# Performance work log

Measured on AMD Instinct MI355X. Metric: run time of the kernel, lower is better.

Reference implementation:

```python
import jax, jax.numpy as jnp
import numpy as np

N_NODES = 100000


def _gcn_conv(x, W, b, src, dst, n):
    # PyG GCNConv (default): add self-loops, norm = deg^{-1/2}[src] * deg^{-1/2}[dst]
    # degree computed on target nodes (col) with unit edge weights, then
    # out[i] = sum_{(j->i)} norm_ji * (x_j @ W) + b
    loops = jnp.arange(n, dtype=src.dtype)
    s = jnp.concatenate([src, loops])
    d = jnp.concatenate([dst, loops])
    deg = jax.ops.segment_sum(jnp.ones_like(d, dtype=x.dtype), d, num_segments=n)
    dinv = jnp.where(deg > 0, jax.lax.rsqrt(deg), 0.0)
    h = x @ W                                  # [n, out_dim]
    norm = (dinv[s] * dinv[d])[:, None]        # [E+n, 1]
    msg = h[s] * norm                          # gather + scale
    out = jax.ops.segment_sum(msg, d, num_segments=n)  # scatter-add to targets
    return out + b


def setup_inputs() -> dict:
    key = jax.random.key(0)
    ks = jax.random.split(key, 4)
    x = jax.random.normal(ks[0], (N_NODES, 128), dtype=jnp.float32)
    edge_index = jax.random.randint(ks[1], (2, 1600000), 0, N_NODES, dtype=jnp.int64)
    W1 = jax.random.normal(ks[2], (128, 16), dtype=jnp.float32) * (1.0 / np.sqrt(128))
    b1 = jnp.zeros((16,), dtype=jnp.float32)
    W2 = jax.random.normal(ks[3], (16, 3), dtype=jnp.float32) * (1.0 / np.sqrt(16))
    b2 = jnp.zeros((3,), dtype=jnp.float32)
    return {"x": x, "edge_index": edge_index, "W1": W1, "b1": b1, "W2": W2, "b2": b2}


def reference(x, edge_index, W1, b1, W2, b2):
    src, dst = edge_index[0], edge_index[1]
    n = x.shape[0]
    h = _gcn_conv(x, W1, b1, src, dst, n)
    h = jax.nn.relu(h)
    # F.dropout in eval mode == identity (deterministic baseline)
    h = _gcn_conv(h, W2, b2, src, dst, n)
    return jax.nn.log_softmax(h, axis=1)
```

## Files before the change

### kernel.cpp

```cpp
#include <hip/hip_runtime.h>
#include <hip/hip_fp16.h>
#include <math.h>


#define BSH 9
#define BNODES 512
#define P1 512
#define GROWS 64
#define K2BUF 10240
#define BCAP 12288
#define EPT 16
#define EPT2 12
#define CSTR 16

struct alignas(8) Half4 { __half x, y, z, w; };

__global__ void k1b_fat(const int* __restrict__ src, const int* __restrict__ dst,
                        int* __restrict__ cursor,
                        unsigned int* __restrict__ staging,
                        const float* __restrict__ x, const float* __restrict__ W1,
                        Half4* __restrict__ g1h, int NBK, int n, int E) {
    __shared__ int smem[7432];
    int b = blockIdx.x;
    int t = threadIdx.x;
    if (b < P1) {
        int* hist  = smem;
        int* cs    = smem + 256;
        int* rbase = smem + 512;
        int* cur   = smem + 768;
        int* buf   = smem + 1024;
        int* gaddr = smem + 4224;
        int* wsum  = smem + 7424;
        hist[t] = 0; cur[t] = 0;
        __syncthreads();
        int slice = (E + P1 - 1) / P1;
        int e0 = b * slice, e1 = min(E, e0 + slice);
        int len = e1 - e0;
        int dl[EPT], sl[EPT];
        int cnt = 0;
        for (int e = e0 + t; e < e1 && cnt < EPT; e += 256, ++cnt) {
            dl[cnt] = dst[e];
            sl[cnt] = src[e];
        }
        for (int i = 0; i < cnt; ++i)
            atomicAdd(&hist[dl[i] >> BSH], 1);
        __syncthreads();
        int h = hist[t];
        int xx = h;
        #pragma unroll
        for (int o = 1; o < 64; o <<= 1) {
            int v = __shfl_up(xx, o);
            if ((t & 63) >= o) xx += v;
        }
        if ((t & 63) == 63) wsum[t >> 6] = xx;
        __syncthreads();
        int wv = t >> 6;
        #pragma unroll
        for (int i = 0; i < 4; ++i)
            if (i < wv) xx += wsum[i];
        cs[t] = xx - h;
        rbase[t] = (h > 0 && t < NBK) ? atomicAdd(&cursor[t * CSTR], h) : 0;
        __syncthreads();
        for (int i = 0; i < cnt; ++i) {
            int d = dl[i], s = sl[i];
            int k = d >> BSH;
            int tk = atomicAdd(&cur[k], 1);
            int pos = cs[k] + tk;
            buf[pos] = (s << BSH) | (d & (BNODES - 1));
            int g = rbase[k] + tk;
            gaddr[pos] = (g < BCAP) ? (k * BCAP + g) : -1;
        }
        __syncthreads();
        for (int p = t; p < len; p += 256) {
            int a = gaddr[p];
            if (a >= 0) staging[a] = (unsigned int)buf[p];
        }
    } else {
        float4* sW4 = (float4*)smem;
        for (int i = t; i < 512; i += 256) sW4[i] = ((const float4*)W1)[i];
        __syncthreads();
        int r = t >> 2, c4 = t & 3;
        int row = (b - P1) * GROWS + r;
        if (row >= n) return;
        float acc[16];
        #pragma unroll
        for (int j = 0; j < 16; ++j) acc[j] = 0.f;
        const float4* xr = (const float4*)(x + (size_t)row * 128);
        #pragma unroll
        for (int q = 0; q < 8; ++q) {
            float4 xv = xr[q * 4 + c4];
            #pragma unroll
            for (int j = 0; j < 4; ++j) {
                int k = q * 16 + c4 * 4 + j;
                float s = (j == 0) ? xv.x : (j == 1) ? xv.y : (j == 2) ? xv.z : xv.w;
                #pragma unroll
                for (int cq = 0; cq < 4; ++cq) {
                    float4 w = sW4[k * 4 + cq];
                    acc[cq * 4 + 0] += s * w.x; acc[cq * 4 + 1] += s * w.y;
                    acc[cq * 4 + 2] += s * w.z; acc[cq * 4 + 3] += s * w.w;
                }
            }
        }
        #pragma unroll
        for (int j = 0; j < 8; ++j) {
            float send = (c4 & 1) ? acc[j] : acc[j + 8];
            float recv = __shfl_xor(send, 1);
            acc[j] = ((c4 & 1) ? acc[j + 8] : acc[j]) + recv;
        }
        #pragma unroll
        for (int j = 0; j < 4; ++j) {
            float send = (c4 & 2) ? acc[j] : acc[j + 4];
            float recv = __shfl_xor(send, 2);
            acc[j] = ((c4 & 2) ? acc[j + 4] : acc[j]) + recv;
        }
        int cidx = 2 * (c4 & 1) + ((c4 & 2) >> 1);
        Half4 hh;
        hh.x = __float2half(acc[0]); hh.y = __float2half(acc[1]);
        hh.z = __float2half(acc[2]); hh.w = __float2half(acc[3]);
        g1h[(size_t)row * 4 + cidx] = hh;
    }
}

__global__ void __launch_bounds__(1024) k2_bucket(
        const unsigned int* __restrict__ staging, const int* __restrict__ cursor,
        int* __restrict__ csr, int* __restrict__ deg, float* __restrict__ dinv,
        int* __restrict__ row_start, Half4* __restrict__ g1h, int n) {
    __shared__ int lh[BNODES], sc[BNODES], lcur[BNODES], wsum[8];
    __shared__ float ldv[BNODES];
    __shared__ int buf[K2BUF];
    int kb = blockIdx.x, t = threadIdx.x;
    int node0 = kb << BSH;
    int nloc = min(BNODES, n - node0);
    int ebase = kb * BCAP;
    int ecnt = min(cursor[kb * CSTR], BCAP);
    if (t < BNODES) { lh[t] = 0; lcur[t] = 0; }
    __syncthreads();
    int el[EPT2];
    int cnt = 0;
    for (int e = t; e < ecnt && cnt < EPT2; e += 1024, ++cnt)
        el[cnt] = (int)staging[ebase + e];
    for (int i = 0; i < cnt; ++i)
        atomicAdd(&lh[el[i] & (BNODES - 1)], 1);
    __syncthreads();
    int own = (t < BNODES) ? lh[t] : 0;
    int xx = own;
    #pragma unroll
    for (int o = 1; o < 64; o <<= 1) {
        int v = __shfl_up(xx, o);
        if ((t & 63) >= o) xx += v;
    }
    if (t < BNODES && (t & 63) == 63) wsum[t >> 6] = xx;
    __syncthreads();
    if (t < BNODES) {
        int wv = t >> 6;
        #pragma unroll
        for (int i = 0; i < 8; ++i)
            if (i < wv) xx += wsum[i];
        int excl = xx - own;
        if (t < nloc) {
            deg[node0 + t] = own;
            row_start[node0 + t] = ebase + excl;
            float dv = rsqrtf((float)(own + 1));
            dinv[node0 + t] = dv;
            ldv[t] = dv;
        }
        sc[t] = excl;
    }
    __syncthreads();
    if (ecnt <= K2BUF) {
        for (int i = 0; i < cnt; ++i) {
            int p = el[i];
            int loc = p & (BNODES - 1);
            int tk = atomicAdd(&lcur[loc], 1);
            buf[sc[loc] + tk] = p >> BSH;
        }
        __syncthreads();
        for (int p = t; p < ecnt; p += 1024)
            csr[ebase + p] = buf[p];
    } else {
        for (int i = 0; i < cnt; ++i) {
            int p = el[i];
            int loc = p & (BNODES - 1);
            int tk = atomicAdd(&lcur[loc], 1);
            csr[ebase + sc[loc] + tk] = p >> BSH;
        }
    }
    for (int j = t; j < nloc * 4; j += 1024) {
        float dv = ldv[j >> 2];
        Half4 v = g1h[(size_t)node0 * 4 + j];
        v.x = __float2half(__half2float(v.x) * dv);
        v.y = __float2half(__half2float(v.y) * dv);
        v.z = __float2half(__half2float(v.z) * dv);
        v.w = __float2half(__half2float(v.w) * dv);
        g1h[(size_t)node0 * 4 + j] = v;
    }
}

__global__ void __launch_bounds__(256, 6) k_gather1(
        const uint4* __restrict__ g1q, const int* __restrict__ csr,
        const int* __restrict__ row_start, const int* __restrict__ deg,
        const float* __restrict__ dinv, const float* __restrict__ b1,
        const float* __restrict__ W2, Half4* __restrict__ g2h, int n) {
    int idx = blockIdx.x * 256 + threadIdx.x;
    int i = idx >> 2, l = idx & 3;
    if (i >= n) return;
    int off = row_start[i], dg = deg[i];
    float acc[16];
    #pragma unroll
    for (int j = 0; j < 16; ++j) acc[j] = 0.f;
    if (l == 0) {
        uint4 p0 = g1q[2 * (size_t)i], p1 = g1q[2 * (size_t)i + 1];
        const __half2* h0 = reinterpret_cast<const __half2*>(&p0);
        const __half2* h1 = reinterpret_cast<const __half2*>(&p1);
        #pragma unroll
        for (int j = 0; j < 4; ++j) {
            float2 f0 = __half22float2(h0[j]);
            float2 f1 = __half22float2(h1[j]);
            acc[2 * j] += f0.x; acc[2 * j + 1] += f0.y;
            acc[8 + 2 * j] += f1.x; acc[9 + 2 * j] += f1.y;
        }
    }
    #pragma unroll 4
    for (int k = l; k < dg; k += 4) {
        int s = csr[off + k];
        uint4 p0 = g1q[2 * (size_t)s], p1 = g1q[2 * (size_t)s + 1];
        const __half2* h0 = reinterpret_cast<const __half2*>(&p0);
        const __half2* h1 = reinterpret_cast<const __half2*>(&p1);
        #pragma unroll
        for (int j = 0; j < 4; ++j) {
            float2 f0 = __half22float2(h0[j]);
            float2 f1 = __half22float2(h1[j]);
            acc[2 * j] += f0.x; acc[2 * j + 1] += f0.y;
            acc[8 + 2 * j] += f1.x; acc[9 + 2 * j] += f1.y;
        }
    }
    #pragma unroll
    for (int j = 0; j < 8; ++j) {
        float send = (l & 1) ? acc[j] : acc[j + 8];
        float recv = __shfl_xor(send, 1);
        acc[j] = ((l & 1) ? acc[j + 8] : acc[j]) + recv;
    }
    #pragma unroll
    for (int j = 0; j < 4; ++j) {
        float send = (l & 2) ? acc[j] : acc[j + 4];
        float recv = __shfl_xor(send, 2);
        acc[j] = ((l & 2) ? acc[j + 4] : acc[j]) + recv;
    }
    int cidx = 2 * (l & 1) + ((l & 2) >> 1);
    float di = dinv[i];
    float o0 = 0.f, o1 = 0.f, o2 = 0.f;
    #pragma unroll
    for (int j = 0; j < 4; ++j) {
        int f = cidx * 4 + j;
        float z = fmaxf(0.f, di * acc[j] + b1[f]);
        o0 += z * W2[f * 3 + 0];
        o1 += z * W2[f * 3 + 1];
        o2 += z * W2[f * 3 + 2];
    }
    o0 += __shfl_xor(o0, 1); o1 += __shfl_xor(o1, 1); o2 += __shfl_xor(o2, 1);
    o0 += __shfl_xor(o0, 2); o1 += __shfl_xor(o1, 2); o2 += __shfl_xor(o2, 2);
    if (l != 0) return;
    Half4 g;
    g.x = __float2half(di * o0); g.y = __float2half(di * o1);
    g.z = __float2half(di * o2); g.w = __float2half(0.f);
    g2h[i] = g;
}

__global__ void __launch_bounds__(256, 6) k_gather2(
        const Half4* __restrict__ g2h, const int* __restrict__ csr,
        const int* __restrict__ row_start, const int* __restrict__ deg,
        const float* __restrict__ dinv, const float* __restrict__ b2,
        float* __restrict__ out, int n) {
    int idx = blockIdx.x * 256 + threadIdx.x;
    int i = idx >> 2, l = idx & 3;
    if (i >= n) return;
    int off = row_start[i], dg = deg[i];
    float v0 = 0.f, v1 = 0.f, v2 = 0.f;
    if (l == 0) {
        Half4 s = g2h[i];
        v0 = __half2float(s.x); v1 = __half2float(s.y); v2 = __half2float(s.z);
    }
    #pragma unroll 4
    for (int e = l; e < dg; e += 4) {
        int s = csr[off + e];
        Half4 g = g2h[s];
        v0 += __half2float(g.x); v1 += __half2float(g.y); v2 += __half2float(g.z);
    }
    v0 += __shfl_xor(v0, 1); v1 += __shfl_xor(v1, 1); v2 += __shfl_xor(v2, 1);
    v0 += __shfl_xor(v0, 2); v1 += __shfl_xor(v1, 2); v2 += __shfl_xor(v2, 2);
    if (l >= 3) return;
    float di = dinv[i];
    float a0 = di * v0 + b2[0];
    float a1 = di * v1 + b2[1];
    float a2 = di * v2 + b2[2];
    float m = fmaxf(a0, fmaxf(a1, a2));
    float lse = logf(expf(a0 - m) + expf(a1 - m) + expf(a2 - m));
    float r = (l == 0) ? a0 : (l == 1) ? a1 : a2;
    out[(size_t)i * 3 + l] = r - m - lse;
}

extern "C" void kernel_launch(void* const* d_in, const int* in_sizes, int n_in,
                              void* d_out, int out_size, void* d_ws, size_t ws_size,
                              hipStream_t stream) {
    const float* x  = (const float*)d_in[0];
    const int*   ei = (const int*)d_in[1];
    const float* W1 = (const float*)d_in[2];
    const float* b1 = (const float*)d_in[3];
    const float* W2 = (const float*)d_in[4];
    const float* b2 = (const float*)d_in[5];
    float* out = (float*)d_out;

    const int n = in_sizes[0] / 128;
    const int E = in_sizes[1] / 2;
    const int* src = ei;
    const int* dst = ei + E;

    const int NBK = (n + BNODES - 1) >> BSH;

    auto align = [](size_t v) { return (v + 255) & ~(size_t)255; };
    char* ws = (char*)d_ws;
    size_t o = 0;
    int* cursor   = (int*)(ws + o); o = align(o + (size_t)NBK * CSTR * 4);
    int* deg      = (int*)(ws + o); o = align(o + (size_t)n * 4);
    float* dinv   = (float*)(ws + o); o = align(o + (size_t)n * 4);
    int* row_start= (int*)(ws + o); o = align(o + (size_t)n * 4);
    unsigned int* staging = (unsigned int*)(ws + o); o = align(o + (size_t)NBK * BCAP * 4);
    int* csr      = (int*)(ws + o); o = align(o + (size_t)NBK * BCAP * 4);
    Half4* g1h    = (Half4*)(ws + o); o = align(o + (size_t)n * 4 * 8);
    Half4* g2h    = (Half4*)(ws + o); o = align(o + (size_t)n * 8);

    const int B = 256;
    int gGemm = (n + GROWS - 1) / GROWS;
    int gn4   = (4 * n + B - 1) / B;

    hipMemsetAsync(cursor, 0, (size_t)NBK * CSTR * 4, stream);
    k1b_fat<<<P1 + gGemm, B, 0, stream>>>(src, dst, cursor, staging,
                                          x, W1, g1h, NBK, n, E);
    k2_bucket<<<NBK, 1024, 0, stream>>>(staging, cursor, csr, deg, dinv, row_start, g1h, n);
    k_gather1<<<gn4, B, 0, stream>>>((const uint4*)g1h, csr, row_start, deg, dinv, b1, W2,
                                     g2h, n);
    k_gather2<<<gn4, B, 0, stream>>>(g2h, csr, row_start, deg, dinv, b2, out, n);
}
```

Baseline: 159.5 us.

## Fuse two gather kernels with a grid-wide atomic barrier

Merges the layer-1 gather/ReLU/W2 projection kernel and the layer-2 gather/log-softmax kernel into one launch. A software grid barrier (an atomic counter zeroed by the existing memset, polled with sleep) separates the two phases, and g2h is written and read with agent-scope atomics so values are visible across blocks. This removes one kernel launch and the drain/refill gap between the two gathers. The barrier is only safe if all ~1563 blocks are co-resident, which is why launch bounds are raised to 8. Otherwise it can deadlock, and the spinning and atomic loads add their own overhead.

```diff
diff --git a/kernel.cpp b/kernel.cpp
--- a/kernel.cpp
+++ b/kernel.cpp
@@ -196,95 +196,104 @@
     }
 }
 
-__global__ void __launch_bounds__(256, 6) k_gather1(
+__global__ void __launch_bounds__(256, 8) k_gather_fused(
         const uint4* __restrict__ g1q, const int* __restrict__ csr,
         const int* __restrict__ row_start, const int* __restrict__ deg,
         const float* __restrict__ dinv, const float* __restrict__ b1,
-        const float* __restrict__ W2, Half4* __restrict__ g2h, int n) {
+        const float* __restrict__ W2, const float* __restrict__ b2,
+        Half4* __restrict__ g2h, float* __restrict__ out,
+        int* __restrict__ bar, int n) {
     int idx = blockIdx.x * 256 + threadIdx.x;
     int i = idx >> 2, l = idx & 3;
-    if (i >= n) return;
-    int off = row_start[i], dg = deg[i];
-    float acc[16];
-    #pragma unroll
-    for (int j = 0; j < 16; ++j) acc[j] = 0.f;
-    if (l == 0) {
-        uint4 p0 = g1q[2 * (size_t)i], p1 = g1q[2 * (size_t)i + 1];
-        const __half2* h0 = reinterpret_cast<const __half2*>(&p0);
-        const __half2* h1 = reinterpret_cast<const __half2*>(&p1);
+    if (i < n) {
+        int off = row_start[i], dg = deg[i];
+        float acc[16];
+        #pragma unroll
+        for (int j = 0; j < 16; ++j) acc[j] = 0.f;
+        if (l == 0) {
+            uint4 p0 = g1q[2 * (size_t)i], p1 = g1q[2 * (size_t)i + 1];
+            const __half2* h0 = reinterpret_cast<const __half2*>(&p0);
+            const __half2* h1 = reinterpret_cast<const __half2*>(&p1);
+            #pragma unroll
+            for (int j = 0; j < 4; ++j) {
+                float2 f0 = __half22float2(h0[j]);
+                float2 f1 = __half22float2(h1[j]);
+                acc[2 * j] += f0.x; acc[2 * j + 1] += f0.y;
+                acc[8 + 2 * j] += f1.x; acc[9 + 2 * j] += f1.y;
+            }
+        }
+        #pragma unroll 4
+        for (int k = l; k < dg; k += 4) {
+            int s = csr[off + k];
+            uint4 p0 = g1q[2 * (size_t)s], p1 = g1q[2 * (size_t)s + 1];
+            const __half2* h0 = reinterpret_cast<const __half2*>(&p0);
+            const __half2* h1 = reinterpret_cast<const __half2*>(&p1);
+            #pragma unroll
+            for (int j = 0; j < 4; ++j) {
+                float2 f0 = __half22float2(h0[j]);
+                float2 f1 = __half22float2(h1[j]);
+                acc[2 * j] += f0.x; acc[2 * j + 1] += f0.y;
+                acc[8 + 2 * j] += f1.x; acc[9 + 2 * j] += f1.y;
+            }
+        }
+        #pragma unroll
+        for (int j = 0; j < 8; ++j) {
+            float send = (l & 1) ? acc[j] : acc[j + 8];
+            float recv = __shfl_xor(send, 1);
+            acc[j] = ((l & 1) ? acc[j + 8] : acc[j]) + recv;
+        }
         #pragma unroll
         for (int j = 0; j < 4; ++j) {
-            float2 f0 = __half22float2(h0[j]);
-            float2 f1 = __half22float2(h1[j]);
-            acc[2 * j] += f0.x; acc[2 * j + 1] += f0.y;
-            acc[8 + 2 * j] += f1.x; acc[9 + 2 * j] += f1.y;
-        }
-    }
-    #pragma unroll 4
-    for (int k = l; k < dg; k += 4) {
-        int s = csr[off + k];
-        uint4 p0 = g1q[2 * (size_t)s], p1 = g1q[2 * (size_t)s + 1];
-        const __half2* h0 = reinterpret_cast<const __half2*>(&p0);
-        const __half2* h1 = reinterpret_cast<const __half2*>(&p1);
+            float send = (l & 2) ? acc[j] : acc[j + 4];
+            float recv = __shfl_xor(send, 2);
+            acc[j] = ((l & 2) ? acc[j + 4] : acc[j]) + recv;
+        }
+        int cidx = 2 * (l & 1) + ((l & 2) >> 1);
+        float di = dinv[i];
+        float o0 = 0.f, o1 = 0.f, o2 = 0.f;
         #pragma unroll
         for (int j = 0; j < 4; ++j) {
-            float2 f0 = __half22float2(h0[j]);
-            float2 f1 = __half22float2(h1[j]);
-            acc[2 * j] += f0.x; acc[2 * j + 1] += f0.y;
-            acc[8 + 2 * j] += f1.x; acc[9 + 2 * j] += f1.y;
-        }
-    }
-    #pragma unroll
-    for (int j = 0; j < 8; ++j) {
-        float send = (l & 1) ? acc[j] : acc[j + 8];
-        float recv = __shfl_xor(send, 1);
-        acc[j] = ((l & 1) ? acc[j + 8] : acc[j]) + recv;
-    }
-    #pragma unroll
-    for (int j = 0; j < 4; ++j) {
-        float send = (l & 2) ? acc[j] : acc[j + 4];
-        float recv = __shfl_xor(send, 2);
-        acc[j] = ((l & 2) ? acc[j + 4] : acc[j]) + recv;
-    }
-    int cidx = 2 * (l & 1) + ((l & 2) >> 1);
-    float di = dinv[i];
-    float o0 = 0.f, o1 = 0.f, o2 = 0.f;
-    #pragma unroll
-    for (int j = 0; j < 4; ++j) {
-        int f = cidx * 4 + j;
-        float z = fmaxf(0.f, di * acc[j] + b1[f]);
-        o0 += z * W2[f * 3 + 0];
-        o1 += z * W2[f * 3 + 1];
-        o2 += z * W2[f * 3 + 2];
-    }
-    o0 += __shfl_xor(o0, 1); o1 += __shfl_xor(o1, 1); o2 += __shfl_xor(o2, 1);
-    o0 += __shfl_xor(o0, 2); o1 += __shfl_xor(o1, 2); o2 += __shfl_xor(o2, 2);
-    if (l != 0) return;
-    Half4 g;
-    g.x = __float2half(di * o0); g.y = __float2half(di * o1);
-    g.z = __float2half(di * o2); g.w = __float2half(0.f);
-    g2h[i] = g;
-}
-
-__global__ void __launch_bounds__(256, 6) k_gather2(
-        const Half4* __restrict__ g2h, const int* __restrict__ csr,
-        const int* __restrict__ row_start, const int* __restrict__ deg,
-        const float* __restrict__ dinv, const float* __restrict__ b2,
-        float* __restrict__ out, int n) {
-    int idx = blockIdx.x * 256 + threadIdx.x;
-    int i = idx >> 2, l = idx & 3;
+            int f = cidx * 4 + j;
+            float z = fmaxf(0.f, di * acc[j] + b1[f]);
+            o0 += z * W2[f * 3 + 0];
+            o1 += z * W2[f * 3 + 1];
+            o2 += z * W2[f * 3 + 2];
+        }
+        o0 += __shfl_xor(o0, 1); o1 += __shfl_xor(o1, 1); o2 += __shfl_xor(o2, 1);
+        o0 += __shfl_xor(o0, 2); o1 += __shfl_xor(o1, 2); o2 += __shfl_xor(o2, 2);
+        if (l == 0) {
+            union { Half4 h; unsigned long long u; } pk;
+            pk.h.x = __float2half(di * o0); pk.h.y = __float2half(di * o1);
+            pk.h.z = __float2half(di * o2); pk.h.w = __float2half(0.f);
+            __hip_atomic_store((unsigned long long*)&g2h[i], pk.u,
+                               __ATOMIC_RELEASE, __HIP_MEMORY_SCOPE_AGENT);
+        }
+    }
+    __syncthreads();
+    if (threadIdx.x == 0) {
+        __threadfence();
+        atomicAdd(bar, 1);
+        while (__hip_atomic_load(bar, __ATOMIC_ACQUIRE,
+                                 __HIP_MEMORY_SCOPE_AGENT) < (int)gridDim.x)
+            __builtin_amdgcn_s_sleep(16);
+    }
+    __syncthreads();
+    __threadfence();
     if (i >= n) return;
     int off = row_start[i], dg = deg[i];
     float v0 = 0.f, v1 = 0.f, v2 = 0.f;
+    union { Half4 h; unsigned long long u; } pk;
     if (l == 0) {
-        Half4 s = g2h[i];
-        v0 = __half2float(s.x); v1 = __half2float(s.y); v2 = __half2float(s.z);
+        pk.u = __hip_atomic_load((const unsigned long long*)&g2h[i],
+                                 __ATOMIC_RELAXED, __HIP_MEMORY_SCOPE_AGENT);
+        v0 = __half2float(pk.h.x); v1 = __half2float(pk.h.y); v2 = __half2float(pk.h.z);
     }
     #pragma unroll 4
     for (int e = l; e < dg; e += 4) {
         int s = csr[off + e];
-        Half4 g = g2h[s];
-        v0 += __half2float(g.x); v1 += __half2float(g.y); v2 += __half2float(g.z);
+        pk.u = __hip_atomic_load((const unsigned long long*)&g2h[s],
+                                 __ATOMIC_RELAXED, __HIP_MEMORY_SCOPE_AGENT);
+        v0 += __half2float(pk.h.x); v1 += __half2float(pk.h.y); v2 += __half2float(pk.h.z);
     }
     v0 += __shfl_xor(v0, 1); v1 += __shfl_xor(v1, 1); v2 += __shfl_xor(v2, 1);
     v0 += __shfl_xor(v0, 2); v1 += __shfl_xor(v1, 2); v2 += __shfl_xor(v2, 2);
@@ -320,7 +329,7 @@
     auto align = [](size_t v) { return (v + 255) & ~(size_t)255; };
     char* ws = (char*)d_ws;
     size_t o = 0;
-    int* cursor   = (int*)(ws + o); o = align(o + (size_t)NBK * CSTR * 4);
+    int* cursor   = (int*)(ws + o); o = align(o + (size_t)NBK * CSTR * 4 + 64);
     int* deg      = (int*)(ws + o); o = align(o + (size_t)n * 4);
     float* dinv   = (float*)(ws + o); o = align(o + (size_t)n * 4);
     int* row_start= (int*)(ws + o); o = align(o + (size_t)n * 4);
@@ -329,15 +338,16 @@
     Half4* g1h    = (Half4*)(ws + o); o = align(o + (size_t)n * 4 * 8);
     Half4* g2h    = (Half4*)(ws + o); o = align(o + (size_t)n * 8);
 
+    int* bar = cursor + NBK * CSTR;
+
     const int B = 256;
     int gGemm = (n + GROWS - 1) / GROWS;
     int gn4   = (4 * n + B - 1) / B;
 
-    hipMemsetAsync(cursor, 0, (size_t)NBK * CSTR * 4, stream);
+    hipMemsetAsync(cursor, 0, (size_t)NBK * CSTR * 4 + 64, stream);
     k1b_fat<<<P1 + gGemm, B, 0, stream>>>(src, dst, cursor, staging,
                                           x, W1, g1h, NBK, n, E);
     k2_bucket<<<NBK, 1024, 0, stream>>>(staging, cursor, csr, deg, dinv, row_start, g1h, n);
-    k_gather1<<<gn4, B, 0, stream>>>((const uint4*)g1h, csr, row_start, deg, dinv, b1, W2,
-                                     g2h, n);
-    k_gather2<<<gn4, B, 0, stream>>>(g2h, csr, row_start, deg, dinv, b2, out, n);
+    k_gather_fused<<<gn4, B, 0, stream>>>((const uint4*)g1h, csr, row_start, deg,
+                                          dinv, b1, W2, b2, g2h, out, bar, n);
 }
```

Result: slower. 611.3 us (+283.2%).

## Replace CSR build and gathers with bucketed shared-memory atomic aggregation

Applied to the files above, without the earlier changes.

Removes the per-bucket CSR construction (prefix scan, local sort, csr/row_start/deg arrays). Instead, each layer's aggregation runs one block per 512-node destination bucket, reading the unsorted staging edges directly and accumulating messages into shared memory with float atomics. The degree kernel now only builds a histogram for dinv and pre-scales g1h. This avoids the CSR write and read traffic and the sorting work, but adds heavy LDS atomic contention (16 atomics per edge in layer 1), runs only about 196 blocks of 1024 threads, and makes the floating-point summation order nondeterministic.

```diff
diff --git a/kernel.cpp b/kernel.cpp
--- a/kernel.cpp
+++ b/kernel.cpp
@@ -7,10 +7,8 @@
 #define BNODES 512
 #define P1 512
 #define GROWS 64
-#define K2BUF 10240
 #define BCAP 12288
 #define EPT 16
-#define EPT2 12
 #define CSTR 16
 
 struct alignas(8) Half4 { __half x, y, z, w; };
@@ -121,71 +119,28 @@
     }
 }
 
-__global__ void __launch_bounds__(1024) k2_bucket(
+__global__ void __launch_bounds__(512) k_deg(
         const unsigned int* __restrict__ staging, const int* __restrict__ cursor,
-        int* __restrict__ csr, int* __restrict__ deg, float* __restrict__ dinv,
-        int* __restrict__ row_start, Half4* __restrict__ g1h, int n) {
-    __shared__ int lh[BNODES], sc[BNODES], lcur[BNODES], wsum[8];
+        float* __restrict__ dinv, Half4* __restrict__ g1h, int n) {
+    __shared__ int hist[BNODES];
     __shared__ float ldv[BNODES];
-    __shared__ int buf[K2BUF];
     int kb = blockIdx.x, t = threadIdx.x;
     int node0 = kb << BSH;
     int nloc = min(BNODES, n - node0);
     int ebase = kb * BCAP;
     int ecnt = min(cursor[kb * CSTR], BCAP);
-    if (t < BNODES) { lh[t] = 0; lcur[t] = 0; }
-    __syncthreads();
-    int el[EPT2];
-    int cnt = 0;
-    for (int e = t; e < ecnt && cnt < EPT2; e += 1024, ++cnt)
-        el[cnt] = (int)staging[ebase + e];
-    for (int i = 0; i < cnt; ++i)
-        atomicAdd(&lh[el[i] & (BNODES - 1)], 1);
-    __syncthreads();
-    int own = (t < BNODES) ? lh[t] : 0;
-    int xx = own;
-    #pragma unroll
-    for (int o = 1; o < 64; o <<= 1) {
-        int v = __shfl_up(xx, o);
-        if ((t & 63) >= o) xx += v;
-    }
-    if (t < BNODES && (t & 63) == 63) wsum[t >> 6] = xx;
+    if (t < BNODES) hist[t] = 0;
+    __syncthreads();
+    for (int e = t; e < ecnt; e += 512)
+        atomicAdd(&hist[staging[ebase + e] & (BNODES - 1)], 1);
     __syncthreads();
     if (t < BNODES) {
-        int wv = t >> 6;
-        #pragma unroll
-        for (int i = 0; i < 8; ++i)
-            if (i < wv) xx += wsum[i];
-        int excl = xx - own;
-        if (t < nloc) {
-            deg[node0 + t] = own;
-            row_start[node0 + t] = ebase + excl;
-            float dv = rsqrtf((float)(own + 1));
-            dinv[node0 + t] = dv;
-            ldv[t] = dv;
-        }
-        sc[t] = excl;
-    }
-    __syncthreads();
-    if (ecnt <= K2BUF) {
-        for (int i = 0; i < cnt; ++i) {
-            int p = el[i];
-            int loc = p & (BNODES - 1);
-            int tk = atomicAdd(&lcur[loc], 1);
-            buf[sc[loc] + tk] = p >> BSH;
-        }
-        __syncthreads();
-        for (int p = t; p < ecnt; p += 1024)
-            csr[ebase + p] = buf[p];
-    } else {
-        for (int i = 0; i < cnt; ++i) {
-            int p = el[i];
-            int loc = p & (BNODES - 1);
-            int tk = atomicAdd(&lcur[loc], 1);
-            csr[ebase + sc[loc] + tk] = p >> BSH;
-        }
-    }
-    for (int j = t; j < nloc * 4; j += 1024) {
+        float dv = rsqrtf((float)(hist[t] + 1));
+        ldv[t] = dv;
+        if (t < nloc) dinv[node0 + t] = dv;
+    }
+    __syncthreads();
+    for (int j = t; j < nloc * 4; j += 512) {
         float dv = ldv[j >> 2];
         Half4 v = g1h[(size_t)node0 * 4 + j];
         v.x = __float2half(__half2float(v.x) * dv);
@@ -196,107 +151,107 @@
     }
 }
 
-__global__ void __launch_bounds__(256, 6) k_gather1(
-        const uint4* __restrict__ g1q, const int* __restrict__ csr,
-        const int* __restrict__ row_start, const int* __restrict__ deg,
-        const float* __restrict__ dinv, const float* __restrict__ b1,
-        const float* __restrict__ W2, Half4* __restrict__ g2h, int n) {
-    int idx = blockIdx.x * 256 + threadIdx.x;
-    int i = idx >> 2, l = idx & 3;
-    if (i >= n) return;
-    int off = row_start[i], dg = deg[i];
-    float acc[16];
-    #pragma unroll
-    for (int j = 0; j < 16; ++j) acc[j] = 0.f;
-    if (l == 0) {
+__global__ void __launch_bounds__(1024) k_l1(
+        const unsigned int* __restrict__ staging, const int* __restrict__ cursor,
+        const uint4* __restrict__ g1q, const float* __restrict__ dinv,
+        const float* __restrict__ b1, const float* __restrict__ W2,
+        Half4* __restrict__ g2h, int n) {
+    __shared__ float acc[BNODES][17];
+    int kb = blockIdx.x, t = threadIdx.x;
+    int node0 = kb << BSH;
+    int nloc = min(BNODES, n - node0);
+    int ebase = kb * BCAP;
+    int ecnt = min(cursor[kb * CSTR], BCAP);
+    for (int j = t; j < BNODES * 17; j += 1024) ((float*)acc)[j] = 0.f;
+    __syncthreads();
+    #pragma unroll 2
+    for (int e = t; e < ecnt; e += 1024) {
+        unsigned int p = staging[ebase + e];
+        int dl = p & (BNODES - 1);
+        int s  = (int)(p >> BSH);
+        uint4 p0 = g1q[2 * (size_t)s], p1 = g1q[2 * (size_t)s + 1];
+        const __half2* h0 = reinterpret_cast<const __half2*>(&p0);
+        const __half2* h1 = reinterpret_cast<const __half2*>(&p1);
+        float* a = acc[dl];
+        #pragma unroll
+        for (int j = 0; j < 4; ++j) {
+            float2 f0 = __half22float2(h0[j]);
+            float2 f1 = __half22float2(h1[j]);
+            atomicAdd(&a[2 * j],     f0.x);
+            atomicAdd(&a[2 * j + 1], f0.y);
+            atomicAdd(&a[8 + 2 * j], f1.x);
+            atomicAdd(&a[9 + 2 * j], f1.y);
+        }
+    }
+    __syncthreads();
+    if (t < nloc) {
+        int i = node0 + t;
+        float dv = dinv[i];
         uint4 p0 = g1q[2 * (size_t)i], p1 = g1q[2 * (size_t)i + 1];
         const __half2* h0 = reinterpret_cast<const __half2*>(&p0);
         const __half2* h1 = reinterpret_cast<const __half2*>(&p1);
+        float v[16];
         #pragma unroll
         for (int j = 0; j < 4; ++j) {
             float2 f0 = __half22float2(h0[j]);
             float2 f1 = __half22float2(h1[j]);
-            acc[2 * j] += f0.x; acc[2 * j + 1] += f0.y;
-            acc[8 + 2 * j] += f1.x; acc[9 + 2 * j] += f1.y;
-        }
-    }
-    #pragma unroll 4
-    for (int k = l; k < dg; k += 4) {
-        int s = csr[off + k];
-        uint4 p0 = g1q[2 * (size_t)s], p1 = g1q[2 * (size_t)s + 1];
-        const __half2* h0 = reinterpret_cast<const __half2*>(&p0);
-        const __half2* h1 = reinterpret_cast<const __half2*>(&p1);
-        #pragma unroll
-        for (int j = 0; j < 4; ++j) {
-            float2 f0 = __half22float2(h0[j]);
-            float2 f1 = __half22float2(h1[j]);
-            acc[2 * j] += f0.x; acc[2 * j + 1] += f0.y;
-            acc[8 + 2 * j] += f1.x; acc[9 + 2 * j] += f1.y;
-        }
-    }
-    #pragma unroll
-    for (int j = 0; j < 8; ++j) {
-        float send = (l & 1) ? acc[j] : acc[j + 8];
-        float recv = __shfl_xor(send, 1);
-        acc[j] = ((l & 1) ? acc[j + 8] : acc[j]) + recv;
-    }
-    #pragma unroll
-    for (int j = 0; j < 4; ++j) {
-        float send = (l & 2) ? acc[j] : acc[j + 4];
-        float recv = __shfl_xor(send, 2);
-        acc[j] = ((l & 2) ? acc[j + 4] : acc[j]) + recv;
-    }
-    int cidx = 2 * (l & 1) + ((l & 2) >> 1);
-    float di = dinv[i];
-    float o0 = 0.f, o1 = 0.f, o2 = 0.f;
-    #pragma unroll
-    for (int j = 0; j < 4; ++j) {
-        int f = cidx * 4 + j;
-        float z = fmaxf(0.f, di * acc[j] + b1[f]);
-        o0 += z * W2[f * 3 + 0];
-        o1 += z * W2[f * 3 + 1];
-        o2 += z * W2[f * 3 + 2];
-    }
-    o0 += __shfl_xor(o0, 1); o1 += __shfl_xor(o1, 1); o2 += __shfl_xor(o2, 1);
-    o0 += __shfl_xor(o0, 2); o1 += __shfl_xor(o1, 2); o2 += __shfl_xor(o2, 2);
-    if (l != 0) return;
-    Half4 g;
-    g.x = __float2half(di * o0); g.y = __float2half(di * o1);
-    g.z = __float2half(di * o2); g.w = __float2half(0.f);
-    g2h[i] = g;
-}
-
-__global__ void __launch_bounds__(256, 6) k_gather2(
-        const Half4* __restrict__ g2h, const int* __restrict__ csr,
-        const int* __restrict__ row_start, const int* __restrict__ deg,
-        const float* __restrict__ dinv, const float* __restrict__ b2,
-        float* __restrict__ out, int n) {
-    int idx = blockIdx.x * 256 + threadIdx.x;
-    int i = idx >> 2, l = idx & 3;
-    if (i >= n) return;
-    int off = row_start[i], dg = deg[i];
-    float v0 = 0.f, v1 = 0.f, v2 = 0.f;
-    if (l == 0) {
-        Half4 s = g2h[i];
-        v0 = __half2float(s.x); v1 = __half2float(s.y); v2 = __half2float(s.z);
-    }
-    #pragma unroll 4
-    for (int e = l; e < dg; e += 4) {
-        int s = csr[off + e];
+            v[2 * j]     = acc[t][2 * j]     + f0.x;
+            v[2 * j + 1] = acc[t][2 * j + 1] + f0.y;
+            v[8 + 2 * j] = acc[t][8 + 2 * j] + f1.x;
+            v[9 + 2 * j] = acc[t][9 + 2 * j] + f1.y;
+        }
+        float o0 = 0.f, o1 = 0.f, o2 = 0.f;
+        #pragma unroll
+        for (int f = 0; f < 16; ++f) {
+            float z = fmaxf(0.f, dv * v[f] + b1[f]);
+            o0 += z * W2[f * 3 + 0];
+            o1 += z * W2[f * 3 + 1];
+            o2 += z * W2[f * 3 + 2];
+        }
+        Half4 g;
+        g.x = __float2half(dv * o0); g.y = __float2half(dv * o1);
+        g.z = __float2half(dv * o2); g.w = __float2half(0.f);
+        g2h[i] = g;
+    }
+}
+
+__global__ void __launch_bounds__(1024) k_l2(
+        const unsigned int* __restrict__ staging, const int* __restrict__ cursor,
+        const Half4* __restrict__ g2h, const float* __restrict__ dinv,
+        const float* __restrict__ b2, float* __restrict__ out, int n) {
+    __shared__ float acc[BNODES][5];
+    int kb = blockIdx.x, t = threadIdx.x;
+    int node0 = kb << BSH;
+    int nloc = min(BNODES, n - node0);
+    int ebase = kb * BCAP;
+    int ecnt = min(cursor[kb * CSTR], BCAP);
+    for (int j = t; j < BNODES * 5; j += 1024) ((float*)acc)[j] = 0.f;
+    __syncthreads();
+    #pragma unroll 2
+    for (int e = t; e < ecnt; e += 1024) {
+        unsigned int p = staging[ebase + e];
+        int dl = p & (BNODES - 1);
+        int s  = (int)(p >> BSH);
         Half4 g = g2h[s];
-        v0 += __half2float(g.x); v1 += __half2float(g.y); v2 += __half2float(g.z);
-    }
-    v0 += __shfl_xor(v0, 1); v1 += __shfl_xor(v1, 1); v2 += __shfl_xor(v2, 1);
-    v0 += __shfl_xor(v0, 2); v1 += __shfl_xor(v1, 2); v2 += __shfl_xor(v2, 2);
-    if (l >= 3) return;
-    float di = dinv[i];
-    float a0 = di * v0 + b2[0];
-    float a1 = di * v1 + b2[1];
-    float a2 = di * v2 + b2[2];
-    float m = fmaxf(a0, fmaxf(a1, a2));
-    float lse = logf(expf(a0 - m) + expf(a1 - m) + expf(a2 - m));
-    float r = (l == 0) ? a0 : (l == 1) ? a1 : a2;
-    out[(size_t)i * 3 + l] = r - m - lse;
+        float* a = acc[dl];
+        atomicAdd(&a[0], __half2float(g.x));
+        atomicAdd(&a[1], __half2float(g.y));
+        atomicAdd(&a[2], __half2float(g.z));
+    }
+    __syncthreads();
+    if (t < nloc) {
+        int i = node0 + t;
+        float dv = dinv[i];
+        Half4 s4 = g2h[i];
+        float a0 = dv * (acc[t][0] + __half2float(s4.x)) + b2[0];
+        float a1 = dv * (acc[t][1] + __half2float(s4.y)) + b2[1];
+        float a2 = dv * (acc[t][2] + __half2float(s4.z)) + b2[2];
+        float m = fmaxf(a0, fmaxf(a1, a2));
+        float lse = logf(expf(a0 - m) + expf(a1 - m) + expf(a2 - m));
+        out[(size_t)i * 3 + 0] = a0 - m - lse;
+        out[(size_t)i * 3 + 1] = a1 - m - lse;
+        out[(size_t)i * 3 + 2] = a2 - m - lse;
+    }
 }
 
 extern "C" void kernel_launch(void* const* d_in, const int* in_sizes, int n_in,
@@ -321,23 +276,19 @@
     char* ws = (char*)d_ws;
     size_t o = 0;
     int* cursor   = (int*)(ws + o); o = align(o + (size_t)NBK * CSTR * 4);
-    int* deg      = (int*)(ws + o); o = align(o + (size_t)n * 4);
     float* dinv   = (float*)(ws + o); o = align(o + (size_t)n * 4);
-    int* row_start= (int*)(ws + o); o = align(o + (size_t)n * 4);
     unsigned int* staging = (unsigned int*)(ws + o); o = align(o + (size_t)NBK * BCAP * 4);
-    int* csr      = (int*)(ws + o); o = align(o + (size_t)NBK * BCAP * 4);
     Half4* g1h    = (Half4*)(ws + o); o = align(o + (size_t)n * 4 * 8);
     Half4* g2h    = (Half4*)(ws + o); o = align(o + (size_t)n * 8);
 
     const int B = 256;
     int gGemm = (n + GROWS - 1) / GROWS;
-    int gn4   = (4 * n + B - 1) / B;
 
     hipMemsetAsync(cursor, 0, (size_t)NBK * CSTR * 4, stream);
     k1b_fat<<<P1 + gGemm, B, 0, stream>>>(src, dst, cursor, staging,
                                           x, W1, g1h, NBK, n, E);
-    k2_bucket<<<NBK, 1024, 0, stream>>>(staging, cursor, csr, deg, dinv, row_start, g1h, n);
-    k_gather1<<<gn4, B, 0, stream>>>((const uint4*)g1h, csr, row_start, deg, dinv, b1, W2,
-                                     g2h, n);
-    k_gather2<<<gn4, B, 0, stream>>>(g2h, csr, row_start, deg, dinv, b2, out, n);
-}
+    k_deg<<<NBK, 512, 0, stream>>>(staging, cursor, dinv, g1h, n);
+    k_l1<<<NBK, 1024, 0, stream>>>(staging, cursor, (const uint4*)g1h, dinv,
+                                   b1, W2, g2h, n);
+    k_l2<<<NBK, 1024, 0, stream>>>(staging, cursor, g2h, dinv, b2, out, n);
+}
```

Result: slower. 340.2 us (+113.3%).

## Halve k2_bucket block size and privatize per-wave-group histograms

Applied to the files above, without the earlier changes.

The bucket-sort kernel now runs 512 threads per block instead of 1024, with each thread handling up to 24 edges instead of 12. The shared histogram is split into four copies, one per 128-thread group, which reduces LDS atomic contention. Per-group prefix offsets are then reused as placement cursors, so the separate lcur array is gone. Shared buffer capacity shrinks to 9216, so more buckets may fall back to the direct global scatter path. It also risks less latency hiding per block.

```diff
diff --git a/kernel.cpp b/kernel.cpp
--- a/kernel.cpp
+++ b/kernel.cpp
@@ -7,10 +7,10 @@
 #define BNODES 512
 #define P1 512
 #define GROWS 64
-#define K2BUF 10240
+#define K2BUF 9216
 #define BCAP 12288
 #define EPT 16
-#define EPT2 12
+#define EPT2 24
 #define CSTR 16
 
 struct alignas(8) Half4 { __half x, y, z, w; };
@@ -121,37 +121,49 @@
     }
 }
 
-__global__ void __launch_bounds__(1024) k2_bucket(
+__global__ void __launch_bounds__(512) k2_bucket(
         const unsigned int* __restrict__ staging, const int* __restrict__ cursor,
         int* __restrict__ csr, int* __restrict__ deg, float* __restrict__ dinv,
         int* __restrict__ row_start, Half4* __restrict__ g1h, int n) {
-    __shared__ int lh[BNODES], sc[BNODES], lcur[BNODES], wsum[8];
+    __shared__ int lh[4][BNODES];
+    __shared__ int sc[BNODES], wsum[8];
     __shared__ float ldv[BNODES];
     __shared__ int buf[K2BUF];
     int kb = blockIdx.x, t = threadIdx.x;
+    int wg = t >> 7;
     int node0 = kb << BSH;
     int nloc = min(BNODES, n - node0);
     int ebase = kb * BCAP;
     int ecnt = min(cursor[kb * CSTR], BCAP);
-    if (t < BNODES) { lh[t] = 0; lcur[t] = 0; }
+    for (int j = t; j < 4 * BNODES; j += 512) ((int*)lh)[j] = 0;
     __syncthreads();
     int el[EPT2];
     int cnt = 0;
-    for (int e = t; e < ecnt && cnt < EPT2; e += 1024, ++cnt)
+    for (int e = t; e < ecnt && cnt < EPT2; e += 512, ++cnt)
         el[cnt] = (int)staging[ebase + e];
     for (int i = 0; i < cnt; ++i)
-        atomicAdd(&lh[el[i] & (BNODES - 1)], 1);
+        atomicAdd(&lh[wg][el[i] & (BNODES - 1)], 1);
     __syncthreads();
-    int own = (t < BNODES) ? lh[t] : 0;
+    int own;
+    {
+        int pg = 0;
+        #pragma unroll
+        for (int g = 0; g < 4; ++g) {
+            int c = lh[g][t];
+            lh[g][t] = pg;
+            pg += c;
+        }
+        own = pg;
+    }
     int xx = own;
     #pragma unroll
     for (int o = 1; o < 64; o <<= 1) {
         int v = __shfl_up(xx, o);
         if ((t & 63) >= o) xx += v;
     }
-    if (t < BNODES && (t & 63) == 63) wsum[t >> 6] = xx;
+    if ((t & 63) == 63) wsum[t >> 6] = xx;
     __syncthreads();
-    if (t < BNODES) {
+    {
         int wv = t >> 6;
         #pragma unroll
         for (int i = 0; i < 8; ++i)
@@ -171,21 +183,21 @@
         for (int i = 0; i < cnt; ++i) {
             int p = el[i];
             int loc = p & (BNODES - 1);
-            int tk = atomicAdd(&lcur[loc], 1);
-            buf[sc[loc] + tk] = p >> BSH;
-        }
-        __syncthreads();
-        for (int p = t; p < ecnt; p += 1024)
+            int ord = atomicAdd(&lh[wg][loc], 1);
+            buf[sc[loc] + ord] = p >> BSH;
+        }
+        __syncthreads();
+        for (int p = t; p < ecnt; p += 512)
             csr[ebase + p] = buf[p];
     } else {
         for (int i = 0; i < cnt; ++i) {
             int p = el[i];
             int loc = p & (BNODES - 1);
-            int tk = atomicAdd(&lcur[loc], 1);
-            csr[ebase + sc[loc] + tk] = p >> BSH;
-        }
-    }
-    for (int j = t; j < nloc * 4; j += 1024) {
+            int ord = atomicAdd(&lh[wg][loc], 1);
+            csr[ebase + sc[loc] + ord] = p >> BSH;
+        }
+    }
+    for (int j = t; j < nloc * 4; j += 512) {
         float dv = ldv[j >> 2];
         Half4 v = g1h[(size_t)node0 * 4 + j];
         v.x = __float2half(__half2float(v.x) * dv);
@@ -336,7 +348,7 @@
     hipMemsetAsync(cursor, 0, (size_t)NBK * CSTR * 4, stream);
     k1b_fat<<<P1 + gGemm, B, 0, stream>>>(src, dst, cursor, staging,
                                           x, W1, g1h, NBK, n, E);
-    k2_bucket<<<NBK, 1024, 0, stream>>>(staging, cursor, csr, deg, dinv, row_start, g1h, n);
+    k2_bucket<<<NBK, 512, 0, stream>>>(staging, cursor, csr, deg, dinv, row_start, g1h, n);
     k_gather1<<<gn4, B, 0, stream>>>((const uint4*)g1h, csr, row_start, deg, dinv, b1, W2,
                                      g2h, n);
     k_gather2<<<gn4, B, 0, stream>>>(g2h, csr, row_start, deg, dinv, b2, out, n);
```

Result: slower. 163.7 us (+2.6%).
